# Optimization experiments

Hardware: AMD Instinct MI355X
Metric: run time of the kernel (lower is better)

## Reference

```python
import jax, jax.numpy as jnp
import numpy as np
from jax import lax

BATCH = 4096
SEQ = 200
VOCAB = 100000
HID = 128


def setup_inputs() -> dict:
    key = jax.random.key(0)
    k0, k1, k2, k3, k4 = jax.random.split(key, 5)
    inputs = jax.random.randint(k0, (BATCH, SEQ), 0, VOCAB, dtype=jnp.int32).astype(jnp.int64)
    emb = jax.random.normal(k1, (VOCAB, HID), dtype=jnp.float32) * 0.05
    # Keras GRU (reset_after=True): kernel [H,3H], recurrent_kernel [H,3H], bias [2,3H]
    kernel = jax.random.normal(k2, (HID, 3 * HID), dtype=jnp.float32) * (1.0 / np.sqrt(HID))
    rec_kernel = jax.random.normal(k3, (HID, 3 * HID), dtype=jnp.float32) * (1.0 / np.sqrt(HID))
    bias = jax.random.normal(k4, (2, 3 * HID), dtype=jnp.float32) * 0.01
    return {"inputs": inputs, "emb": emb, "kernel": kernel, "rec_kernel": rec_kernel, "bias": bias}


def _masked_gru(x, mask, kernel, rec_kernel, bias):
    # x: [B,S,H] embedded inputs; mask: [B,S] bool (True = valid timestep)
    input_bias, rec_bias = bias[0], bias[1]
    # Precompute all input projections in one big GEMM: [B,S,3H]
    xproj = jnp.einsum('bsh,hk->bsk', x, kernel) + input_bias
    B, H = x.shape[0], x.shape[2]

    def step(h, scan_in):
        xp, m = scan_in  # xp: [B,3H], m: [B]
        hp = h @ rec_kernel + rec_bias  # [B,3H]
        xz, xr, xh = xp[:, :H], xp[:, H:2 * H], xp[:, 2 * H:]
        hz, hr, hh_rec = hp[:, :H], hp[:, H:2 * H], hp[:, 2 * H:]
        z = jax.nn.sigmoid(xz + hz)
        r = jax.nn.sigmoid(xr + hr)
        hh = jnp.tanh(xh + r * hh_rec)  # reset_after=True: r applied after recurrent matmul
        h_new = z * h + (1.0 - z) * hh
        # mask_zero semantics: masked steps carry previous state through
        h_new = jnp.where(m[:, None], h_new, h)
        return h_new, None

    h0 = jnp.zeros((B, H), dtype=x.dtype)
    xs = (jnp.swapaxes(xproj, 0, 1), jnp.swapaxes(mask, 0, 1))  # time-major
    h_final, _ = lax.scan(step, h0, xs)
    return h_final  # [B,H] == last valid-step output under Keras masking


def reference(inputs, emb, kernel, rec_kernel, bias):
    x = emb[inputs]              # [B,S,H] embedding lookup
    mask = inputs != 0           # mask_zero=True
    return _masked_gru(x, mask, kernel, rec_kernel, bias)
```

## Files before the change

### kernel.cpp

```cpp
#include <hip/hip_runtime.h>

#define BATCH 4096
#define SEQ   200
#define HID   128
#define ROWS  16
#define NTH   512

typedef _Float16 f16;
typedef f16 f16x4 __attribute__((ext_vector_type(4)));
typedef f16 f16x8 __attribute__((ext_vector_type(8)));
typedef float f32x4 __attribute__((ext_vector_type(4)));

#define MFMA(a, b, c) __builtin_amdgcn_mfma_f32_16x16x32_f16((a), (b), (c), 0, 0, 0)

__device__ __forceinline__ float fast_exp2(float x) {
#if defined(__has_builtin) && __has_builtin(__builtin_amdgcn_exp2f)
    return __builtin_amdgcn_exp2f(x);
#else
    float r; asm volatile("v_exp_f32 %0, %1\n\ts_nop 0" : "=v"(r) : "v"(x)); return r;
#endif
}
__device__ __forceinline__ float fast_rcp(float x) {
#if defined(__has_builtin) && __has_builtin(__builtin_amdgcn_rcpf)
    return __builtin_amdgcn_rcpf(x);
#else
    float r; asm volatile("v_rcp_f32 %0, %1\n\ts_nop 0" : "=v"(r) : "v"(x)); return r;
#endif
}
#define LOG2E  1.442695041f
#define LOG2E2 2.885390082f

__global__ __attribute__((amdgpu_flat_work_group_size(NTH, NTH)))
void gru_mfma(const int* __restrict__ inputs,
              const float* __restrict__ emb,
              const float* __restrict__ kernel,
              const float* __restrict__ rec_kernel,
              const float* __restrict__ bias,
              float* __restrict__ out)
{
    __shared__ __align__(16) f16 xb[2][4][64][8];
    __shared__ __align__(16) f16 hb[2][4][64][8];
    __shared__ int tok_sh[2][ROWS];
    __shared__ int ts_sh;

    const int tid  = threadIdx.x;
    const int lane = tid & 63;
    const int j0   = (tid >> 6) * 16;
    const int l15  = lane & 15;
    const int hi   = lane >> 4;
    const int r0   = hi * 4;
    const int row0 = blockIdx.x * ROWS;

    if (tid == 0) { int any = 0; for (int i = 1; i < 128; i += 2) any |= inputs[i]; ts_sh = any ? 1 : 2; }

    f16x8 Bx[3][4];
    f16x8 Brz[4], Brr[4], Brh[4];
    const float gsc[3] = { -LOG2E, -LOG2E, LOG2E2 };
#pragma unroll
    for (int g = 0; g < 3; ++g)
#pragma unroll
        for (int kt = 0; kt < 4; ++kt) {
            f16x8 t;
#pragma unroll
            for (int e = 0; e < 8; ++e)
                t[e] = (f16)(gsc[g] * kernel[(size_t)(kt * 32 + hi * 8 + e) * 384 + g * HID + j0 + l15]);
            Bx[g][kt] = t;
        }
#pragma unroll
    for (int kt = 0; kt < 4; ++kt) {
        f16x8 tz, tr, th;
#pragma unroll
        for (int e = 0; e < 8; ++e) {
            const size_t krow = (size_t)(kt * 32 + hi * 8 + e) * 384;
            tz[e] = (f16)(-LOG2E  * rec_kernel[krow + j0 + l15]);
            tr[e] = (f16)(-LOG2E  * rec_kernel[krow + HID + j0 + l15]);
            th[e] = (f16)(LOG2E2 * rec_kernel[krow + 2 * HID + j0 + l15]);
        }
        Brz[kt] = tz; Brr[kt] = tr; Brh[kt] = th;
    }

    f32x4 bzv, brv, bxhv, brhv;
#pragma unroll
    for (int i = 0; i < 4; ++i) {
        const int c = j0 + r0 + i;
        bzv[i]  = -LOG2E * (bias[c]       + bias[384 + c]);
        brv[i]  = -LOG2E * (bias[128 + c] + bias[512 + c]);
        bxhv[i] =  LOG2E2 * bias[256 + c];
        brhv[i] =  LOG2E2 * bias[640 + c];
    }

    f32x4 h = {0.f, 0.f, 0.f, 0.f};

    const int hk  = j0 + r0;
    const int hwi = (((hk >> 5) * 64) + (((hk & 31) >> 3) * 16) + l15) * 8 + (hk & 7);

    const int skt  = tid >> 7;
    const int sidx = tid & 127;
    const int su   = sidx >> 1;
    const int shalf= sidx & 1;
    const int sb   = su & 15;
    const int shid = skt * 32 + (su >> 4) * 8 + shalf * 4;
    const int sw   = ((size_t)0, (skt * 64 + su) * 8 + shalf * 4);
    const bool twr = (tid < 32) && ((tid & 1) == 0);

    for (int i = tid; i < 4 * 64 * 8; i += NTH) ((f16*)hb)[i] = (f16)0.f;
    __syncthreads();
    const int ts = ts_sh;

    {
        const int tok0 = inputs[((size_t)(row0 + sb) * SEQ + 0) * ts];
        if (twr) tok_sh[0][sb] = tok0;
        const float4 v = *(const float4*)&emb[(size_t)tok0 * HID + shid];
        f16x4 xv; xv[0] = (f16)v.x; xv[1] = (f16)v.y; xv[2] = (f16)v.z; xv[3] = (f16)v.w;
        *(f16x4*)&((f16*)xb)[sw] = xv;
    }
    int tokA = inputs[((size_t)(row0 + sb) * SEQ + 1) * ts];
    __syncthreads();

    for (int s = 0; s < SEQ; ++s) {
        const int cur = s & 1, nxt = cur ^ 1;
        const bool pf = (s + 1 < SEQ);
        float4 pv; int tokB = tokA;
        if (pf) {
            pv = *(const float4*)&emb[(size_t)tokA * HID + shid];
            const int s2 = (s + 2 < SEQ) ? (s + 2) : (SEQ - 1);
            tokB = inputs[((size_t)(row0 + sb) * SEQ + s2) * ts];
        }

        const int tkk = tok_sh[cur][l15];

        f32x4 azh = {0.f, 0.f, 0.f, 0.f}, arh = {0.f, 0.f, 0.f, 0.f};
        f32x4 ah  = brhv;
#pragma unroll
        for (int kt = 0; kt < 4; ++kt) {
            const f16x8 hB = *(const f16x8*)&hb[cur][kt][lane][0];
            azh = MFMA(Brz[kt], hB, azh);
            arh = MFMA(Brr[kt], hB, arh);
            ah  = MFMA(Brh[kt], hB, ah);
        }
        f32x4 azx = bzv, arx = brv, ax = bxhv;
#pragma unroll
        for (int kt = 0; kt < 4; ++kt) {
            const f16x8 xB = *(const f16x8*)&xb[cur][kt][lane][0];
            azx = MFMA(Bx[0][kt], xB, azx);
            arx = MFMA(Bx[1][kt], xB, arx);
            ax  = MFMA(Bx[2][kt], xB, ax);
        }

        f16x4 hv;
#pragma unroll
        for (int i = 0; i < 4; ++i) {
            const float z  = fast_rcp(1.f + fast_exp2(azx[i] + azh[i]));
            const float rg = fast_rcp(1.f + fast_exp2(arx[i] + arh[i]));
            const float u  = ax[i] + rg * ah[i];
            const float hh = 1.f - 2.f * fast_rcp(1.f + fast_exp2(u));
            const float hn = hh + z * (h[i] - hh);
            h[i] = (tkk != 0) ? hn : h[i];
            hv[i] = (f16)h[i];
        }

        *(f16x4*)&((f16*)hb)[nxt * (4 * 64 * 8) + hwi] = hv;
        if (pf) {
            f16x4 xv; xv[0] = (f16)pv.x; xv[1] = (f16)pv.y; xv[2] = (f16)pv.z; xv[3] = (f16)pv.w;
            *(f16x4*)&((f16*)xb)[nxt * (4 * 64 * 8) + sw] = xv;
            if (twr) tok_sh[nxt][sb] = tokA;
            tokA = tokB;
        }
        __syncthreads();
    }

    float4 o; o.x = h[0]; o.y = h[1]; o.z = h[2]; o.w = h[3];
    *(float4*)&out[(size_t)(row0 + l15) * HID + j0 + r0] = o;
}

extern "C" void kernel_launch(void* const* d_in, const int* in_sizes, int n_in,
                              void* d_out, int out_size, void* d_ws, size_t ws_size,
                              hipStream_t stream) {
    const int* inputs      = (const int*)d_in[0];
    const float* emb       = (const float*)d_in[1];
    const float* kernel    = (const float*)d_in[2];
    const float* rec_k     = (const float*)d_in[3];
    const float* bias      = (const float*)d_in[4];
    float* out             = (float*)d_out;
    gru_mfma<<<BATCH / ROWS, NTH, 0, stream>>>(inputs, emb, kernel, rec_k, bias, out);
}
```

Measured before the change: 171.1 us.

## Compute next step's input projection after the hidden-state update to shorten the critical path

The input-projection MFMAs for step s+1 now run after the hidden state for step s is written, so each step only has the recurrent MFMAs on its critical path. The input projection is accumulated straight into the gate accumulators. The x buffer becomes a triple-buffered ring, and token/embedding prefetch moves one step further ahead. This adds register pressure from the carried accumulators and one more shared-memory buffer, and makes the ring-index bookkeeping more involved.

After: 166.7 us, median of 2. 2.5% less time.

```diff
diff --git a/kernel.cpp b/kernel.cpp
--- a/kernel.cpp
+++ b/kernel.cpp
@@ -38,7 +38,7 @@
               const float* __restrict__ bias,
               float* __restrict__ out)
 {
-    __shared__ __align__(16) f16 xb[2][4][64][8];
+    __shared__ __align__(16) f16 xb[3][4][64][8];
     __shared__ __align__(16) f16 hb[2][4][64][8];
     __shared__ int tok_sh[2][ROWS];
     __shared__ int ts_sh;
@@ -100,59 +100,66 @@
     const int shalf= sidx & 1;
     const int sb   = su & 15;
     const int shid = skt * 32 + (su >> 4) * 8 + shalf * 4;
-    const int sw   = ((size_t)0, (skt * 64 + su) * 8 + shalf * 4);
+    const int sw   = (skt * 64 + su) * 8 + shalf * 4;
     const bool twr = (tid < 32) && ((tid & 1) == 0);
 
     for (int i = tid; i < 4 * 64 * 8; i += NTH) ((f16*)hb)[i] = (f16)0.f;
     __syncthreads();
     const int ts = ts_sh;
 
+    const size_t tbase = (size_t)(row0 + sb) * SEQ;
+    const int tok0 = inputs[(tbase + 0) * ts];
+    int t1 = inputs[(tbase + 1) * ts];
+    int t2 = inputs[(tbase + 2) * ts];
+    if (twr) tok_sh[0][sb] = tok0;
     {
-        const int tok0 = inputs[((size_t)(row0 + sb) * SEQ + 0) * ts];
-        if (twr) tok_sh[0][sb] = tok0;
-        const float4 v = *(const float4*)&emb[(size_t)tok0 * HID + shid];
-        f16x4 xv; xv[0] = (f16)v.x; xv[1] = (f16)v.y; xv[2] = (f16)v.z; xv[3] = (f16)v.w;
-        *(f16x4*)&((f16*)xb)[sw] = xv;
-    }
-    int tokA = inputs[((size_t)(row0 + sb) * SEQ + 1) * ts];
+        const float4 v0 = *(const float4*)&emb[(size_t)tok0 * HID + shid];
+        const float4 v1 = *(const float4*)&emb[(size_t)t1   * HID + shid];
+        f16x4 a; a[0] = (f16)v0.x; a[1] = (f16)v0.y; a[2] = (f16)v0.z; a[3] = (f16)v0.w;
+        f16x4 b; b[0] = (f16)v1.x; b[1] = (f16)v1.y; b[2] = (f16)v1.z; b[3] = (f16)v1.w;
+        *(f16x4*)&((f16*)xb)[sw] = a;
+        *(f16x4*)&((f16*)xb)[1 * (4 * 64 * 8) + sw] = b;
+    }
     __syncthreads();
 
+    f32x4 azx = bzv, arx = brv, axc = bxhv;
+#pragma unroll
+    for (int kt = 0; kt < 4; ++kt) {
+        const f16x8 xB = *(const f16x8*)&xb[0][kt][lane][0];
+        azx = MFMA(Bx[0][kt], xB, azx);
+        arx = MFMA(Bx[1][kt], xB, arx);
+        axc = MFMA(Bx[2][kt], xB, axc);
+    }
+
+    int rd_x = 1, wr_x = 2;
     for (int s = 0; s < SEQ; ++s) {
         const int cur = s & 1, nxt = cur ^ 1;
-        const bool pf = (s + 1 < SEQ);
-        float4 pv; int tokB = tokA;
-        if (pf) {
-            pv = *(const float4*)&emb[(size_t)tokA * HID + shid];
-            const int s2 = (s + 2 < SEQ) ? (s + 2) : (SEQ - 1);
-            tokB = inputs[((size_t)(row0 + sb) * SEQ + s2) * ts];
+        const bool pf1 = (s + 1 < SEQ);
+        const bool pf2 = (s + 2 < SEQ);
+        float4 pv; int t3 = t2;
+        if (pf2) {
+            pv = *(const float4*)&emb[(size_t)t2 * HID + shid];
+            const int s3 = (s + 3 < SEQ) ? (s + 3) : (SEQ - 1);
+            t3 = inputs[(tbase + s3) * ts];
         }
 
         const int tkk = tok_sh[cur][l15];
 
-        f32x4 azh = {0.f, 0.f, 0.f, 0.f}, arh = {0.f, 0.f, 0.f, 0.f};
-        f32x4 ah  = brhv;
+        f32x4 az = azx, ar = arx, ah = brhv;
 #pragma unroll
         for (int kt = 0; kt < 4; ++kt) {
             const f16x8 hB = *(const f16x8*)&hb[cur][kt][lane][0];
-            azh = MFMA(Brz[kt], hB, azh);
-            arh = MFMA(Brr[kt], hB, arh);
-            ah  = MFMA(Brh[kt], hB, ah);
-        }
-        f32x4 azx = bzv, arx = brv, ax = bxhv;
-#pragma unroll
-        for (int kt = 0; kt < 4; ++kt) {
-            const f16x8 xB = *(const f16x8*)&xb[cur][kt][lane][0];
-            azx = MFMA(Bx[0][kt], xB, azx);
-            arx = MFMA(Bx[1][kt], xB, arx);
-            ax  = MFMA(Bx[2][kt], xB, ax);
+            az = MFMA(Brz[kt], hB, az);
+            ar = MFMA(Brr[kt], hB, ar);
+            ah = MFMA(Brh[kt], hB, ah);
         }
 
         f16x4 hv;
 #pragma unroll
         for (int i = 0; i < 4; ++i) {
-            const float z  = fast_rcp(1.f + fast_exp2(azx[i] + azh[i]));
-            const float rg = fast_rcp(1.f + fast_exp2(arx[i] + arh[i]));
-            const float u  = ax[i] + rg * ah[i];
+            const float z  = fast_rcp(1.f + fast_exp2(az[i]));
+            const float rg = fast_rcp(1.f + fast_exp2(ar[i]));
+            const float u  = axc[i] + rg * ah[i];
             const float hh = 1.f - 2.f * fast_rcp(1.f + fast_exp2(u));
             const float hn = hh + z * (h[i] - hh);
             h[i] = (tkk != 0) ? hn : h[i];
@@ -160,12 +167,25 @@
         }
 
         *(f16x4*)&((f16*)hb)[nxt * (4 * 64 * 8) + hwi] = hv;
-        if (pf) {
+
+        if (pf1) {
+            azx = bzv; arx = brv; axc = bxhv;
+#pragma unroll
+            for (int kt = 0; kt < 4; ++kt) {
+                const f16x8 xB = *(const f16x8*)&xb[rd_x][kt][lane][0];
+                azx = MFMA(Bx[0][kt], xB, azx);
+                arx = MFMA(Bx[1][kt], xB, arx);
+                axc = MFMA(Bx[2][kt], xB, axc);
+            }
+            if (twr) tok_sh[nxt][sb] = t1;
+        }
+        if (pf2) {
             f16x4 xv; xv[0] = (f16)pv.x; xv[1] = (f16)pv.y; xv[2] = (f16)pv.z; xv[3] = (f16)pv.w;
-            *(f16x4*)&((f16*)xb)[nxt * (4 * 64 * 8) + sw] = xv;
-            if (twr) tok_sh[nxt][sb] = tokA;
-            tokA = tokB;
-        }
+            *(f16x4*)&((f16*)xb)[wr_x * (4 * 64 * 8) + sw] = xv;
+        }
+        t1 = t2; t2 = t3;
+        rd_x = (rd_x == 2) ? 0 : rd_x + 1;
+        wr_x = (wr_x == 2) ? 0 : wr_x + 1;
         __syncthreads();
     }
 
```
